# Kernel optimization log

Measured on AMD Instinct MI355X. Metric: run time of the kernel, lower is better.

Reference implementation:

```python
import jax, jax.numpy as jnp
import numpy as np

B = 8192
N_COLS = 64
D = 1024
EPS = 1e-5


def _layernorm(x, g, b):
    m = jnp.mean(x, axis=-1, keepdims=True)
    v = jnp.mean(jnp.square(x - m), axis=-1, keepdims=True)
    return (x - m) * jax.lax.rsqrt(v + EPS) * g + b


def setup_inputs() -> dict:
    key = jax.random.key(0)
    ks = jax.random.split(key, 8)
    s = 0.02
    return {
        "x1_enc": jax.random.normal(ks[0], (1, N_COLS, D), jnp.float32),
        "x2_enc": jax.random.normal(ks[1], (B, D), jnp.float32),
        "We": jax.random.normal(ks[2], (4, 2 * D, D), jnp.float32) * s,
        "be": jnp.zeros((4, D), jnp.float32),
        "W1": jax.random.normal(ks[3], (2 * D, 4 * D), jnp.float32) * s,
        "b1": jnp.zeros((4 * D,), jnp.float32),
        "g1": jnp.ones((4 * D,), jnp.float32),
        "bt1": jnp.zeros((4 * D,), jnp.float32),
        "W2": jax.random.normal(ks[4], (4 * D, 2 * D), jnp.float32) * s,
        "b2": jnp.zeros((2 * D,), jnp.float32),
        "g2": jnp.ones((2 * D,), jnp.float32),
        "bt2": jnp.zeros((2 * D,), jnp.float32),
        "W3": jax.random.normal(ks[5], (2 * D, 1), jnp.float32) * s,
        "b3": jnp.zeros((1,), jnp.float32),
        "col_pairs": jax.random.randint(ks[6], (B, 2), 0, N_COLS, jnp.int64),
        "vis_type": jax.random.randint(ks[7], (B,), 0, 4, jnp.int64),
    }


def reference(x1_enc, x2_enc, We, be, W1, b1, g1, bt1, W2, b2, g2, bt2, W3, b3,
              col_pairs, vis_type):
    # x1 repeated B times is identical per row -> gather directly from x1_enc[0]
    x11 = x1_enc[0, col_pairs[:, 0]]          # [B, D]
    x12 = x1_enc[0, col_pairs[:, 1]]          # [B, D]
    x1c = jnp.concatenate([x11, x12], axis=1)  # [B, 2D]

    # 1-of-4 expert routing: compute all experts, select by vis_type
    all_y = jax.nn.relu(jnp.einsum('bd,edk->bek', x1c, We) + be)  # [B, 4, D]
    y1 = jnp.take_along_axis(all_y, vis_type[:, None, None], axis=1)[:, 0]  # [B, D]

    y = jnp.concatenate([y1, x2_enc], axis=1)  # [B, 2D]
    h = _layernorm(jax.nn.relu(y @ W1 + b1), g1, bt1)
    h = _layernorm(jax.nn.relu(h @ W2 + b2), g2, bt2)
    return jax.nn.sigmoid(h @ W3 + b3)  # [B, 1]
```

## Files before the change

kernel.cpp:

```cpp
#include <hip/hip_runtime.h>

typedef unsigned short u16;
typedef __bf16 bf16x8 __attribute__((ext_vector_type(8)));
typedef float f32x4v __attribute__((ext_vector_type(4)));
typedef u16 u16x8 __attribute__((ext_vector_type(8)));

__device__ __forceinline__ u16 f2bf(float f) {
  union { float f; unsigned u; } v; v.f = f;
  unsigned r = v.u + 0x7fffu + ((v.u >> 16) & 1u);
  return (u16)(r >> 16);
}
__device__ __forceinline__ float bf2f(u16 h) {
  union { unsigned u; float f; } v; v.u = ((unsigned)h) << 16;
  return v.f;
}

#define G2L16(g, l)                                                            \
  __builtin_amdgcn_global_load_lds((__attribute__((address_space(1))) void*)(g), \
                                   (__attribute__((address_space(3))) void*)(l), 16, 0, 0)

__global__ __launch_bounds__(256) void k_transpose2(const float* __restrict__ W1,
                                                    u16* __restrict__ W1T,
                                                    const float* __restrict__ W2,
                                                    u16* __restrict__ W2gT,
                                                    const float* __restrict__ g1) {
  __shared__ float tile[64][65];
  int bid = blockIdx.x;
  const float* in;
  u16* out;
  int R, C, bx, by, fold;
  if (bid < 2048) {
    in = W1; out = W1T; R = 2048; C = 4096; fold = 0;
    bx = bid & 63; by = bid >> 6;
  } else {
    bid -= 2048;
    in = W2; out = W2gT; R = 4096; C = 2048; fold = 1;
    bx = bid & 31; by = bid >> 5;
  }
  const int c0 = bx * 64, r0 = by * 64;
  const int tc = (threadIdx.x & 15) * 4, tr = threadIdx.x >> 4;
#pragma unroll
  for (int i = 0; i < 4; ++i) {
    int r = tr + i * 16;
    f32x4v v = *(const f32x4v*)(in + (size_t)(r0 + r) * C + c0 + tc);
    tile[r][tc] = v[0]; tile[r][tc + 1] = v[1];
    tile[r][tc + 2] = v[2]; tile[r][tc + 3] = v[3];
  }
  __syncthreads();
  const int oc = threadIdx.x >> 2;
  const int rb = (threadIdx.x & 3) * 16;
  float gv[16];
#pragma unroll
  for (int i = 0; i < 16; ++i) gv[i] = fold ? g1[r0 + rb + i] : 1.f;
  u16x8 o0, o1;
#pragma unroll
  for (int i = 0; i < 8; ++i) o0[i] = f2bf(tile[rb + i][oc] * gv[i]);
#pragma unroll
  for (int i = 0; i < 8; ++i) o1[i] = f2bf(tile[rb + 8 + i][oc] * gv[8 + i]);
  *(u16x8*)(out + (size_t)(c0 + oc) * R + r0 + rb) = o0;
  *(u16x8*)(out + (size_t)(c0 + oc) * R + r0 + rb + 8) = o1;
}

__global__ __launch_bounds__(256) void k_pq(const float* __restrict__ x1,
                                            const float* __restrict__ We,
                                            float* __restrict__ pq0,
                                            float* __restrict__ pq1) {
  const int n0 = blockIdx.x * 64;
  const int ep = blockIdx.y;
  const int e = ep >> 1, p = ep & 1;
  const int ks = blockIdx.z * 512;
  float* pq = blockIdx.z ? pq1 : pq0;
  __shared__ float As[64][33];
  __shared__ float Bs[32][68];
  const int t = threadIdx.x;
  const int tx = t & 15, ty = t >> 4;
  float acc[4][4] = {};
  const float* wbase = We + (size_t)e * 2048 * 1024 + (size_t)p * 1024 * 1024;
  for (int k0 = ks; k0 < ks + 512; k0 += 32) {
#pragma unroll
    for (int i = 0; i < 8; ++i) {
      int idx = t + i * 256;
      As[idx >> 5][idx & 31] = x1[(size_t)(idx >> 5) * 1024 + k0 + (idx & 31)];
    }
#pragma unroll
    for (int i = 0; i < 8; ++i) {
      int idx = t + i * 256;
      Bs[idx >> 6][idx & 63] = wbase[(size_t)(k0 + (idx >> 6)) * 1024 + n0 + (idx & 63)];
    }
    __syncthreads();
#pragma unroll
    for (int kk = 0; kk < 32; ++kk) {
      float av[4];
#pragma unroll
      for (int i = 0; i < 4; ++i) av[i] = As[ty * 4 + i][kk];
      f32x4v bv = *(const f32x4v*)&Bs[kk][tx * 4];
#pragma unroll
      for (int i = 0; i < 4; ++i)
#pragma unroll
        for (int j = 0; j < 4; ++j) acc[i][j] += av[i] * bv[j];
    }
    __syncthreads();
  }
#pragma unroll
  for (int i = 0; i < 4; ++i) {
    float* dst = pq + ((size_t)ep * 64 + ty * 4 + i) * 1024 + n0 + tx * 4;
#pragma unroll
    for (int j = 0; j < 4; ++j) dst[j] = acc[i][j];
  }
}

__global__ __launch_bounds__(256) void k_w2vec(const float* __restrict__ W2,
                                               const float* __restrict__ g1,
                                               const float* __restrict__ bt1,
                                               const float* __restrict__ b2,
                                               float* __restrict__ s1,
                                               float* __restrict__ c1b) {
  const int n = blockIdx.x * 256 + threadIdx.x;
  const int ks = blockIdx.y * 256;
  float s = 0.f, c = 0.f;
  for (int k = ks; k < ks + 256; ++k) {
    float w = W2[(size_t)k * 2048 + n];
    s += g1[k] * w;
    c += bt1[k] * w;
  }
  if (blockIdx.y == 0) c += b2[n];
  atomicAdd(&s1[n], s);
  atomicAdd(&c1b[n], c);
}

__global__ __launch_bounds__(256) void k_build_y(const float* __restrict__ pq0,
                                                 const float* __restrict__ pq1,
                                                 const float* __restrict__ x2,
                                                 const float* __restrict__ be,
                                                 const int* __restrict__ cp,
                                                 const int* __restrict__ vis,
                                                 u16* __restrict__ Y) {
  const int b = blockIdx.x;
  const int t = threadIdx.x;
  const int e = vis[b];
  u16x8 o;
  if (t < 128) {
    const int c0 = cp[2 * b], c1 = cp[2 * b + 1];
    const size_t po = ((size_t)(e * 2) * 64 + c0) * 1024 + t * 8;
    const size_t qo = ((size_t)(e * 2 + 1) * 64 + c1) * 1024 + t * 8;
    const float* B = be + e * 1024 + t * 8;
#pragma unroll
    for (int i = 0; i < 8; ++i) {
      float v = pq0[po + i] + pq1[po + i] + pq0[qo + i] + pq1[qo + i] + B[i];
      o[i] = f2bf(v > 0.f ? v : 0.f);
    }
    *(u16x8*)(Y + (size_t)b * 2048 + t * 8) = o;
  } else {
    const float* X = x2 + (size_t)b * 1024 + (size_t)(t - 128) * 8;
#pragma unroll
    for (int i = 0; i < 8; ++i) o[i] = f2bf(X[i]);
    *(u16x8*)(Y + (size_t)b * 2048 + 1024 + (size_t)(t - 128) * 8) = o;
  }
}

template <int MODE>
__global__ __launch_bounds__(256, 4) void k_gemm(const u16* __restrict__ A,
                                                 const u16* __restrict__ BT,
                                                 const float* __restrict__ bias,
                                                 const float2* __restrict__ stats,
                                                 const float* __restrict__ s1,
                                                 const float* __restrict__ c1b,
                                                 u16* __restrict__ C, int M, int N, int K) {
  __shared__ u16 As[128 * 64];
  __shared__ u16 Bs[128 * 64];
  const int tid = threadIdx.x;
  const int lane = tid & 63;
  const int wave = tid >> 6;

  const int nx = gridDim.x, ny = gridDim.y;
  const int bid = blockIdx.y * nx + blockIdx.x;
  const int stripe = ny >> 3;
  const int xcd = bid & 7;
  const int loc = bid >> 3;
  const int panel = loc / (stripe * 4);
  const int rem = loc - panel * (stripe * 4);
  const int by = xcd * stripe + (rem >> 2);
  const int bx = panel * 4 + (rem & 3);
  const int tileN = bx * 128;
  const int tileM = by * 128;
  const int wm = wave & 1;
  const int wn = wave >> 1;

  f32x4v acc[4][4];
#pragma unroll
  for (int i = 0; i < 4; ++i)
#pragma unroll
    for (int j = 0; j < 4; ++j) acc[i][j] = (f32x4v){0.f, 0.f, 0.f, 0.f};

  const int srow = tid >> 3;
  const int lchunk = (tid & 7) ^ (srow & 7);
  const u16* aptr = A + (size_t)(tileM + srow) * K + lchunk * 8;
  const u16* bptr = BT + (size_t)(tileN + srow) * K + lchunk * 8;
  u16* asp = As + tid * 8;
  u16* bsp = Bs + tid * 8;

  const int s = lane & 7;
  const int kp0 = ((lane >> 4) ^ s) * 8;
  const int kp1 = kp0 ^ 32;
  const int am = wm * 64 + (lane & 15);
  const int bn = wn * 64 + (lane & 15);

  for (int k0 = 0; k0 < K; k0 += 64) {
    G2L16(aptr, asp);
    G2L16(aptr + (size_t)32 * K, asp + 2048);
    G2L16(aptr + (size_t)64 * K, asp + 4096);
    G2L16(aptr + (size_t)96 * K, asp + 6144);
    G2L16(bptr, bsp);
    G2L16(bptr + (size_t)32 * K, bsp + 2048);
    G2L16(bptr + (size_t)64 * K, bsp + 4096);
    G2L16(bptr + (size_t)96 * K, bsp + 6144);
    aptr += 64;
    bptr += 64;
    __syncthreads();

    bf16x8 af[4], bfr[4];
#pragma unroll
    for (int mi = 0; mi < 4; ++mi)
      af[mi] = *(const bf16x8*)(As + (am + mi * 16) * 64 + kp0);
#pragma unroll
    for (int ni = 0; ni < 4; ++ni)
      bfr[ni] = *(const bf16x8*)(Bs + (bn + ni * 16) * 64 + kp0);
#pragma unroll
    for (int mi = 0; mi < 4; ++mi)
#pragma unroll
      for (int ni = 0; ni < 4; ++ni)
        acc[mi][ni] = __builtin_amdgcn_mfma_f32_16x16x32_bf16(af[mi], bfr[ni], acc[mi][ni], 0, 0, 0);
#pragma unroll
    for (int mi = 0; mi < 4; ++mi)
      af[mi] = *(const bf16x8*)(As + (am + mi * 16) * 64 + kp1);
#pragma unroll
    for (int ni = 0; ni < 4; ++ni)
      bfr[ni] = *(const bf16x8*)(Bs + (bn + ni * 16) * 64 + kp1);
#pragma unroll
    for (int mi = 0; mi < 4; ++mi)
#pragma unroll
      for (int ni = 0; ni < 4; ++ni)
        acc[mi][ni] = __builtin_amdgcn_mfma_f32_16x16x32_bf16(af[mi], bfr[ni], acc[mi][ni], 0, 0, 0);
    __syncthreads();
  }

  const int crow = tileM + wm * 64 + (lane >> 4) * 4;
  const int ccol = tileN + wn * 64 + (lane & 15);
  float cv0[4], cv1[4];
#pragma unroll
  for (int ni = 0; ni < 4; ++ni) {
    const int c = ccol + ni * 16;
    if (MODE == 0) {
      cv0[ni] = bias[c];
    } else {
      cv0[ni] = s1[c];
      cv1[ni] = c1b[c];
    }
  }
#pragma unroll
  for (int mi = 0; mi < 4; ++mi) {
#pragma unroll
    for (int r = 0; r < 4; ++r) {
      const int row = crow + mi * 16 + r;
      float m = 0.f, rs = 0.f;
      if (MODE == 1) {
        float2 st = stats[row];
        m = st.x; rs = st.y;
      }
#pragma unroll
      for (int ni = 0; ni < 4; ++ni) {
        float v;
        if (MODE == 0)
          v = acc[mi][ni][r] + cv0[ni];
        else
          v = rs * acc[mi][ni][r] - rs * m * cv0[ni] + cv1[ni];
        v = v > 0.f ? v : 0.f;
        C[(size_t)row * N + ccol + ni * 16] = f2bf(v);
      }
    }
  }
}

__global__ __launch_bounds__(256) void k_stats(const u16* __restrict__ H1,
                                               float2* __restrict__ stats) {
  const u16* row = H1 + (size_t)blockIdx.x * 4096;
  const int t = threadIdx.x;
  float s = 0.f, ss = 0.f;
#pragma unroll
  for (int j = 0; j < 2; ++j) {
    u16x8 v = *(const u16x8*)(row + j * 2048 + t * 8);
#pragma unroll
    for (int i = 0; i < 8; ++i) {
      float f = bf2f(v[i]);
      s += f;
      ss += f * f;
    }
  }
#pragma unroll
  for (int off = 32; off > 0; off >>= 1) {
    s += __shfl_down(s, off, 64);
    ss += __shfl_down(ss, off, 64);
  }
  __shared__ float red[8];
  const int lane = t & 63, wv = t >> 6;
  if (lane == 0) { red[wv] = s; red[4 + wv] = ss; }
  __syncthreads();
  if (t == 0) {
    float S = red[0] + red[1] + red[2] + red[3];
    float SS = red[4] + red[5] + red[6] + red[7];
    float m = S * (1.f / 4096.f);
    float var = SS * (1.f / 4096.f) - m * m;
    stats[blockIdx.x] = make_float2(m, rsqrtf(var + 1e-5f));
  }
}

__global__ __launch_bounds__(256) void k_ln_final(const u16* __restrict__ H2,
                                                  const float* __restrict__ g,
                                                  const float* __restrict__ bt,
                                                  const float* __restrict__ W3,
                                                  const float* __restrict__ b3,
                                                  float* __restrict__ out) {
  const int b = blockIdx.x, t = threadIdx.x;
  const u16* row = H2 + (size_t)b * 2048;
  float vals[8];
  float s = 0.f, ss = 0.f;
  {
    u16x8 v = *(const u16x8*)(row + t * 8);
#pragma unroll
    for (int i = 0; i < 8; ++i) {
      float f = bf2f(v[i]);
      vals[i] = f;
      s += f;
      ss += f * f;
    }
  }
#pragma unroll
  for (int off = 32; off > 0; off >>= 1) {
    s += __shfl_down(s, off, 64);
    ss += __shfl_down(ss, off, 64);
  }
  __shared__ float red[8];
  const int lane = t & 63, wv = t >> 6;
  if (lane == 0) { red[wv] = s; red[4 + wv] = ss; }
  __syncthreads();
  if (t == 0) {
    float S = red[0] + red[1] + red[2] + red[3];
    float SS = red[4] + red[5] + red[6] + red[7];
    float m = S * (1.f / 2048.f);
    float var = SS * (1.f / 2048.f) - m * m;
    red[0] = m;
    red[1] = rsqrtf(var + 1e-5f);
  }
  __syncthreads();
  const float m = red[0], rs = red[1];
  float dot = 0.f;
#pragma unroll
  for (int i = 0; i < 8; ++i) {
    int col = t * 8 + i;
    float h = (vals[i] - m) * rs * g[col] + bt[col];
    dot += h * W3[col];
  }
#pragma unroll
  for (int off = 32; off > 0; off >>= 1) dot += __shfl_down(dot, off, 64);
  __syncthreads();
  if (lane == 0) red[wv] = dot;
  __syncthreads();
  if (t == 0) {
    float S = red[0] + red[1] + red[2] + red[3] + b3[0];
    out[b] = 1.f / (1.f + expf(-S));
  }
}

extern "C" void kernel_launch(void* const* d_in, const int* in_sizes, int n_in,
                              void* d_out, int out_size, void* d_ws, size_t ws_size,
                              hipStream_t stream) {
  const float* x1 = (const float*)d_in[0];
  const float* x2 = (const float*)d_in[1];
  const float* We = (const float*)d_in[2];
  const float* be = (const float*)d_in[3];
  const float* W1 = (const float*)d_in[4];
  const float* b1 = (const float*)d_in[5];
  const float* g1 = (const float*)d_in[6];
  const float* bt1 = (const float*)d_in[7];
  const float* W2 = (const float*)d_in[8];
  const float* b2 = (const float*)d_in[9];
  const float* g2 = (const float*)d_in[10];
  const float* bt2 = (const float*)d_in[11];
  const float* W3 = (const float*)d_in[12];
  const float* b3 = (const float*)d_in[13];
  const int* cp = (const int*)d_in[14];
  const int* vis = (const int*)d_in[15];
  float* out = (float*)d_out;

  char* ws = (char*)d_ws;
  u16* W1T  = (u16*)(ws);
  u16* W2gT = (u16*)(ws + 16777216);
  u16* Y    = (u16*)(ws + 33554432);
  u16* H1   = (u16*)(ws + 67108864);
  float* PQ0 = (float*)(ws + 134217728);
  float* PQ1 = (float*)(ws + 136314880);
  float2* stats = (float2*)(ws + 138412032);
  float* s1  = (float*)(ws + 138477568);
  float* c1b = (float*)(ws + 138485760);
  u16* H2 = Y;

  hipMemsetAsync(s1, 0, 2 * 2048 * sizeof(float), stream);
  k_transpose2<<<4096, 256, 0, stream>>>(W1, W1T, W2, W2gT, g1);
  k_pq<<<dim3(16, 8, 2), 256, 0, stream>>>(x1, We, PQ0, PQ1);
  k_w2vec<<<dim3(8, 16), 256, 0, stream>>>(W2, g1, bt1, b2, s1, c1b);
  k_build_y<<<8192, 256, 0, stream>>>(PQ0, PQ1, x2, be, cp, vis, Y);
  k_gemm<0><<<dim3(4096 / 128, 8192 / 128), 256, 0, stream>>>(
      Y, W1T, b1, nullptr, nullptr, nullptr, H1, 8192, 4096, 2048);
  k_stats<<<8192, 256, 0, stream>>>(H1, stats);
  k_gemm<1><<<dim3(2048 / 128, 8192 / 128), 256, 0, stream>>>(
      H1, W2gT, nullptr, stats, s1, c1b, H2, 8192, 2048, 4096);
  k_ln_final<<<8192, 256, 0, stream>>>(H2, g2, bt2, W3, b3, out);
}
```

Before: 491.7 us.

## Double-buffer GEMM LDS, fuse LN1 stats and W2 vector sums into producers

The GEMM main loop now uses two LDS buffers, so the next K-tile's global-to-LDS loads are in flight while the current tile is computed. This halves the barriers per tile but doubles shared memory, and the occupancy hint is dropped. Row sum and sum-of-squares for the first layernorm are computed in the GEMM0 epilogue and reduced by a small kernel, replacing the separate pass over H1. The W2·g1 and W2·bt1 vector products are folded into the transpose kernel, and build_y and ln_final process several rows per block with wave-level reductions.

```diff
diff --git a/kernel.cpp b/kernel.cpp
--- a/kernel.cpp
+++ b/kernel.cpp
@@ -23,7 +23,10 @@
                                                     u16* __restrict__ W1T,
                                                     const float* __restrict__ W2,
                                                     u16* __restrict__ W2gT,
-                                                    const float* __restrict__ g1) {
+                                                    const float* __restrict__ g1,
+                                                    const float* __restrict__ bt1,
+                                                    float* __restrict__ w2ps,
+                                                    float* __restrict__ w2pc) {
   __shared__ float tile[64][65];
   int bid = blockIdx.x;
   const float* in;
@@ -38,7 +41,8 @@
     bx = bid & 31; by = bid >> 5;
   }
   const int c0 = bx * 64, r0 = by * 64;
-  const int tc = (threadIdx.x & 15) * 4, tr = threadIdx.x >> 4;
+  const int t = threadIdx.x;
+  const int tc = (t & 15) * 4, tr = t >> 4;
 #pragma unroll
   for (int i = 0; i < 4; ++i) {
     int r = tr + i * 16;
@@ -47,8 +51,8 @@
     tile[r][tc + 2] = v[2]; tile[r][tc + 3] = v[3];
   }
   __syncthreads();
-  const int oc = threadIdx.x >> 2;
-  const int rb = (threadIdx.x & 3) * 16;
+  const int oc = t >> 2;
+  const int rb = (t & 3) * 16;
   float gv[16];
 #pragma unroll
   for (int i = 0; i < 16; ++i) gv[i] = fold ? g1[r0 + rb + i] : 1.f;
@@ -59,6 +63,21 @@
   for (int i = 0; i < 8; ++i) o1[i] = f2bf(tile[rb + 8 + i][oc] * gv[8 + i]);
   *(u16x8*)(out + (size_t)(c0 + oc) * R + r0 + rb) = o0;
   *(u16x8*)(out + (size_t)(c0 + oc) * R + r0 + rb + 8) = o1;
+  if (fold) {
+    float ps = 0.f, pc = 0.f;
+#pragma unroll
+    for (int i = 0; i < 16; ++i) {
+      float w = tile[rb + i][oc];
+      ps += gv[i] * w;
+      pc += bt1[r0 + rb + i] * w;
+    }
+    ps += __shfl_down(ps, 2, 4); ps += __shfl_down(ps, 1, 4);
+    pc += __shfl_down(pc, 2, 4); pc += __shfl_down(pc, 1, 4);
+    if ((t & 3) == 0) {
+      w2ps[(size_t)by * 2048 + c0 + oc] = ps;
+      w2pc[(size_t)by * 2048 + c0 + oc] = pc;
+    }
+  }
 }
 
 __global__ __launch_bounds__(256) void k_pq(const float* __restrict__ x1,
@@ -109,25 +128,6 @@
   }
 }
 
-__global__ __launch_bounds__(256) void k_w2vec(const float* __restrict__ W2,
-                                               const float* __restrict__ g1,
-                                               const float* __restrict__ bt1,
-                                               const float* __restrict__ b2,
-                                               float* __restrict__ s1,
-                                               float* __restrict__ c1b) {
-  const int n = blockIdx.x * 256 + threadIdx.x;
-  const int ks = blockIdx.y * 256;
-  float s = 0.f, c = 0.f;
-  for (int k = ks; k < ks + 256; ++k) {
-    float w = W2[(size_t)k * 2048 + n];
-    s += g1[k] * w;
-    c += bt1[k] * w;
-  }
-  if (blockIdx.y == 0) c += b2[n];
-  atomicAdd(&s1[n], s);
-  atomicAdd(&c1b[n], c);
-}
-
 __global__ __launch_bounds__(256) void k_build_y(const float* __restrict__ pq0,
                                                  const float* __restrict__ pq1,
                                                  const float* __restrict__ x2,
@@ -135,39 +135,78 @@
                                                  const int* __restrict__ cp,
                                                  const int* __restrict__ vis,
                                                  u16* __restrict__ Y) {
-  const int b = blockIdx.x;
   const int t = threadIdx.x;
-  const int e = vis[b];
-  u16x8 o;
-  if (t < 128) {
-    const int c0 = cp[2 * b], c1 = cp[2 * b + 1];
-    const size_t po = ((size_t)(e * 2) * 64 + c0) * 1024 + t * 8;
-    const size_t qo = ((size_t)(e * 2 + 1) * 64 + c1) * 1024 + t * 8;
-    const float* B = be + e * 1024 + t * 8;
-#pragma unroll
-    for (int i = 0; i < 8; ++i) {
-      float v = pq0[po + i] + pq1[po + i] + pq0[qo + i] + pq1[qo + i] + B[i];
-      o[i] = f2bf(v > 0.f ? v : 0.f);
-    }
-    *(u16x8*)(Y + (size_t)b * 2048 + t * 8) = o;
-  } else {
-    const float* X = x2 + (size_t)b * 1024 + (size_t)(t - 128) * 8;
-#pragma unroll
-    for (int i = 0; i < 8; ++i) o[i] = f2bf(X[i]);
-    *(u16x8*)(Y + (size_t)b * 2048 + 1024 + (size_t)(t - 128) * 8) = o;
-  }
-}
+  for (int rr = 0; rr < 8; ++rr) {
+    const int b = blockIdx.x * 8 + rr;
+    const int e = vis[b];
+    u16x8 o;
+    if (t < 128) {
+      const int c0 = cp[2 * b], c1 = cp[2 * b + 1];
+      const size_t po = ((size_t)(e * 2) * 64 + c0) * 1024 + t * 8;
+      const size_t qo = ((size_t)(e * 2 + 1) * 64 + c1) * 1024 + t * 8;
+      const float* B = be + e * 1024 + t * 8;
+#pragma unroll
+      for (int i = 0; i < 8; ++i) {
+        float v = pq0[po + i] + pq1[po + i] + pq0[qo + i] + pq1[qo + i] + B[i];
+        o[i] = f2bf(v > 0.f ? v : 0.f);
+      }
+      *(u16x8*)(Y + (size_t)b * 2048 + t * 8) = o;
+    } else {
+      const float* X = x2 + (size_t)b * 1024 + (size_t)(t - 128) * 8;
+#pragma unroll
+      for (int i = 0; i < 8; ++i) o[i] = f2bf(X[i]);
+      *(u16x8*)(Y + (size_t)b * 2048 + 1024 + (size_t)(t - 128) * 8) = o;
+    }
+  }
+}
+
+#define LOADAB(ASP, BSP)                                                       \
+  {                                                                            \
+    G2L16(aA, (ASP));                                                          \
+    G2L16(aA + (size_t)32 * K, (ASP) + 2048);                                  \
+    G2L16(aA + (size_t)64 * K, (ASP) + 4096);                                  \
+    G2L16(aA + (size_t)96 * K, (ASP) + 6144);                                  \
+    G2L16(bB, (BSP));                                                          \
+    G2L16(bB + (size_t)32 * K, (BSP) + 2048);                                  \
+    G2L16(bB + (size_t)64 * K, (BSP) + 4096);                                  \
+    G2L16(bB + (size_t)96 * K, (BSP) + 6144);                                  \
+    aA += 64; bB += 64;                                                        \
+  }
+
+#define COMPUTE(ASB, BSB)                                                      \
+  {                                                                            \
+    bf16x8 af[4], bfr[4];                                                      \
+    _Pragma("unroll") for (int mi = 0; mi < 4; ++mi)                           \
+        af[mi] = *(const bf16x8*)((ASB) + (am + mi * 16) * 64 + kp0);          \
+    _Pragma("unroll") for (int ni = 0; ni < 4; ++ni)                           \
+        bfr[ni] = *(const bf16x8*)((BSB) + (bn + ni * 16) * 64 + kp0);         \
+    _Pragma("unroll") for (int mi = 0; mi < 4; ++mi)                           \
+        _Pragma("unroll") for (int ni = 0; ni < 4; ++ni)                       \
+            acc[mi][ni] = __builtin_amdgcn_mfma_f32_16x16x32_bf16(             \
+                af[mi], bfr[ni], acc[mi][ni], 0, 0, 0);                        \
+    _Pragma("unroll") for (int mi = 0; mi < 4; ++mi)                           \
+        af[mi] = *(const bf16x8*)((ASB) + (am + mi * 16) * 64 + kp1);          \
+    _Pragma("unroll") for (int ni = 0; ni < 4; ++ni)                           \
+        bfr[ni] = *(const bf16x8*)((BSB) + (bn + ni * 16) * 64 + kp1);         \
+    _Pragma("unroll") for (int mi = 0; mi < 4; ++mi)                           \
+        _Pragma("unroll") for (int ni = 0; ni < 4; ++ni)                       \
+            acc[mi][ni] = __builtin_amdgcn_mfma_f32_16x16x32_bf16(             \
+                af[mi], bfr[ni], acc[mi][ni], 0, 0, 0);                        \
+  }
 
 template <int MODE>
-__global__ __launch_bounds__(256, 4) void k_gemm(const u16* __restrict__ A,
-                                                 const u16* __restrict__ BT,
-                                                 const float* __restrict__ bias,
-                                                 const float2* __restrict__ stats,
-                                                 const float* __restrict__ s1,
-                                                 const float* __restrict__ c1b,
-                                                 u16* __restrict__ C, int M, int N, int K) {
-  __shared__ u16 As[128 * 64];
-  __shared__ u16 Bs[128 * 64];
+__global__ __launch_bounds__(256) void k_gemm(const u16* __restrict__ A,
+                                              const u16* __restrict__ BT,
+                                              const float* __restrict__ bias,
+                                              const float2* __restrict__ stats,
+                                              const float* __restrict__ s1,
+                                              const float* __restrict__ c1b,
+                                              float2* __restrict__ sp_out,
+                                              u16* __restrict__ C, int M, int N, int K) {
+  __shared__ u16 As0[128 * 64];
+  __shared__ u16 As1[128 * 64];
+  __shared__ u16 Bs0[128 * 64];
+  __shared__ u16 Bs1[128 * 64];
   const int tid = threadIdx.x;
   const int lane = tid & 63;
   const int wave = tid >> 6;
@@ -194,10 +233,12 @@
 
   const int srow = tid >> 3;
   const int lchunk = (tid & 7) ^ (srow & 7);
-  const u16* aptr = A + (size_t)(tileM + srow) * K + lchunk * 8;
-  const u16* bptr = BT + (size_t)(tileN + srow) * K + lchunk * 8;
-  u16* asp = As + tid * 8;
-  u16* bsp = Bs + tid * 8;
+  const u16* aA = A + (size_t)(tileM + srow) * K + lchunk * 8;
+  const u16* bB = BT + (size_t)(tileN + srow) * K + lchunk * 8;
+  u16* asp0 = As0 + tid * 8;
+  u16* asp1 = As1 + tid * 8;
+  u16* bsp0 = Bs0 + tid * 8;
+  u16* bsp1 = Bs1 + tid * 8;
 
   const int s = lane & 7;
   const int kp0 = ((lane >> 4) ^ s) * 8;
@@ -205,42 +246,15 @@
   const int am = wm * 64 + (lane & 15);
   const int bn = wn * 64 + (lane & 15);
 
-  for (int k0 = 0; k0 < K; k0 += 64) {
-    G2L16(aptr, asp);
-    G2L16(aptr + (size_t)32 * K, asp + 2048);
-    G2L16(aptr + (size_t)64 * K, asp + 4096);
-    G2L16(aptr + (size_t)96 * K, asp + 6144);
-    G2L16(bptr, bsp);
-    G2L16(bptr + (size_t)32 * K, bsp + 2048);
-    G2L16(bptr + (size_t)64 * K, bsp + 4096);
-    G2L16(bptr + (size_t)96 * K, bsp + 6144);
-    aptr += 64;
-    bptr += 64;
+  const int n = K >> 6;
+  LOADAB(asp0, bsp0);
+  __syncthreads();
+  for (int it = 0; it < n; it += 2) {
+    LOADAB(asp1, bsp1);
+    COMPUTE(As0, Bs0);
     __syncthreads();
-
-    bf16x8 af[4], bfr[4];
-#pragma unroll
-    for (int mi = 0; mi < 4; ++mi)
-      af[mi] = *(const bf16x8*)(As + (am + mi * 16) * 64 + kp0);
-#pragma unroll
-    for (int ni = 0; ni < 4; ++ni)
-      bfr[ni] = *(const bf16x8*)(Bs + (bn + ni * 16) * 64 + kp0);
-#pragma unroll
-    for (int mi = 0; mi < 4; ++mi)
-#pragma unroll
-      for (int ni = 0; ni < 4; ++ni)
-        acc[mi][ni] = __builtin_amdgcn_mfma_f32_16x16x32_bf16(af[mi], bfr[ni], acc[mi][ni], 0, 0, 0);
-#pragma unroll
-    for (int mi = 0; mi < 4; ++mi)
-      af[mi] = *(const bf16x8*)(As + (am + mi * 16) * 64 + kp1);
-#pragma unroll
-    for (int ni = 0; ni < 4; ++ni)
-      bfr[ni] = *(const bf16x8*)(Bs + (bn + ni * 16) * 64 + kp1);
-#pragma unroll
-    for (int mi = 0; mi < 4; ++mi)
-#pragma unroll
-      for (int ni = 0; ni < 4; ++ni)
-        acc[mi][ni] = __builtin_amdgcn_mfma_f32_16x16x32_bf16(af[mi], bfr[ni], acc[mi][ni], 0, 0, 0);
+    if (it + 2 < n) LOADAB(asp0, bsp0);
+    COMPUTE(As1, Bs1);
     __syncthreads();
   }
 
@@ -257,6 +271,7 @@
       cv1[ni] = c1b[c];
     }
   }
+  const int cb = bx * 2 + wn;
 #pragma unroll
   for (int mi = 0; mi < 4; ++mi) {
 #pragma unroll
@@ -267,6 +282,7 @@
         float2 st = stats[row];
         m = st.x; rs = st.y;
       }
+      float s_ = 0.f, ss_ = 0.f;
 #pragma unroll
       for (int ni = 0; ni < 4; ++ni) {
         float v;
@@ -275,42 +291,49 @@
         else
           v = rs * acc[mi][ni][r] - rs * m * cv0[ni] + cv1[ni];
         v = v > 0.f ? v : 0.f;
+        if (MODE == 0) { s_ += v; ss_ += v * v; }
         C[(size_t)row * N + ccol + ni * 16] = f2bf(v);
       }
-    }
-  }
-}
-
-__global__ __launch_bounds__(256) void k_stats(const u16* __restrict__ H1,
-                                               float2* __restrict__ stats) {
-  const u16* row = H1 + (size_t)blockIdx.x * 4096;
-  const int t = threadIdx.x;
-  float s = 0.f, ss = 0.f;
-#pragma unroll
-  for (int j = 0; j < 2; ++j) {
-    u16x8 v = *(const u16x8*)(row + j * 2048 + t * 8);
-#pragma unroll
-    for (int i = 0; i < 8; ++i) {
-      float f = bf2f(v[i]);
-      s += f;
-      ss += f * f;
-    }
-  }
-#pragma unroll
-  for (int off = 32; off > 0; off >>= 1) {
-    s += __shfl_down(s, off, 64);
-    ss += __shfl_down(ss, off, 64);
-  }
-  __shared__ float red[8];
-  const int lane = t & 63, wv = t >> 6;
-  if (lane == 0) { red[wv] = s; red[4 + wv] = ss; }
-  __syncthreads();
-  if (t == 0) {
-    float S = red[0] + red[1] + red[2] + red[3];
-    float SS = red[4] + red[5] + red[6] + red[7];
-    float m = S * (1.f / 4096.f);
-    float var = SS * (1.f / 4096.f) - m * m;
-    stats[blockIdx.x] = make_float2(m, rsqrtf(var + 1e-5f));
+      if (MODE == 0) {
+#pragma unroll
+        for (int off = 8; off >= 1; off >>= 1) {
+          s_ += __shfl_xor(s_, off, 16);
+          ss_ += __shfl_xor(ss_, off, 16);
+        }
+        if ((lane & 15) == 0)
+          sp_out[(size_t)cb * 8192 + row] = make_float2(s_, ss_);
+      }
+    }
+  }
+}
+
+__global__ __launch_bounds__(256) void k_reduce(const float2* __restrict__ sp,
+                                                float2* __restrict__ stats,
+                                                const float* __restrict__ w2ps,
+                                                const float* __restrict__ w2pc,
+                                                const float* __restrict__ b2,
+                                                float* __restrict__ s1,
+                                                float* __restrict__ c1b) {
+  const int bid = blockIdx.x;
+  if (bid < 32) {
+    const int row = bid * 256 + threadIdx.x;
+    float s = 0.f, ss = 0.f;
+    for (int cbk = 0; cbk < 64; ++cbk) {
+      float2 p = sp[(size_t)cbk * 8192 + row];
+      s += p.x; ss += p.y;
+    }
+    float m = s * (1.f / 4096.f);
+    float var = ss * (1.f / 4096.f) - m * m;
+    stats[row] = make_float2(m, rsqrtf(var + 1e-5f));
+  } else {
+    const int nn = (bid - 32) * 256 + threadIdx.x;
+    float s = 0.f, c = 0.f;
+    for (int kb = 0; kb < 64; ++kb) {
+      s += w2ps[(size_t)kb * 2048 + nn];
+      c += w2pc[(size_t)kb * 2048 + nn];
+    }
+    s1[nn] = s;
+    c1b[nn] = c + b2[nn];
   }
 }
 
@@ -320,16 +343,18 @@
                                                   const float* __restrict__ W3,
                                                   const float* __restrict__ b3,
                                                   float* __restrict__ out) {
-  const int b = blockIdx.x, t = threadIdx.x;
+  const int lane = threadIdx.x & 63;
+  const int b = blockIdx.x * 4 + (threadIdx.x >> 6);
   const u16* row = H2 + (size_t)b * 2048;
-  float vals[8];
+  float vals[4][8];
   float s = 0.f, ss = 0.f;
-  {
-    u16x8 v = *(const u16x8*)(row + t * 8);
+#pragma unroll
+  for (int c = 0; c < 4; ++c) {
+    u16x8 v = *(const u16x8*)(row + c * 512 + lane * 8);
 #pragma unroll
     for (int i = 0; i < 8; ++i) {
       float f = bf2f(v[i]);
-      vals[i] = f;
+      vals[c][i] = f;
       s += f;
       ss += f * f;
     }
@@ -339,36 +364,22 @@
     s += __shfl_down(s, off, 64);
     ss += __shfl_down(ss, off, 64);
   }
-  __shared__ float red[8];
-  const int lane = t & 63, wv = t >> 6;
-  if (lane == 0) { red[wv] = s; red[4 + wv] = ss; }
-  __syncthreads();
-  if (t == 0) {
-    float S = red[0] + red[1] + red[2] + red[3];
-    float SS = red[4] + red[5] + red[6] + red[7];
-    float m = S * (1.f / 2048.f);
-    float var = SS * (1.f / 2048.f) - m * m;
-    red[0] = m;
-    red[1] = rsqrtf(var + 1e-5f);
-  }
-  __syncthreads();
-  const float m = red[0], rs = red[1];
+  s = __shfl(s, 0);
+  ss = __shfl(ss, 0);
+  const float m = s * (1.f / 2048.f);
+  const float rs = rsqrtf(ss * (1.f / 2048.f) - m * m + 1e-5f);
   float dot = 0.f;
 #pragma unroll
-  for (int i = 0; i < 8; ++i) {
-    int col = t * 8 + i;
-    float h = (vals[i] - m) * rs * g[col] + bt[col];
-    dot += h * W3[col];
-  }
+  for (int c = 0; c < 4; ++c)
+#pragma unroll
+    for (int i = 0; i < 8; ++i) {
+      int col = c * 512 + lane * 8 + i;
+      float h = (vals[c][i] - m) * rs * g[col] + bt[col];
+      dot += h * W3[col];
+    }
 #pragma unroll
   for (int off = 32; off > 0; off >>= 1) dot += __shfl_down(dot, off, 64);
-  __syncthreads();
-  if (lane == 0) red[wv] = dot;
-  __syncthreads();
-  if (t == 0) {
-    float S = red[0] + red[1] + red[2] + red[3] + b3[0];
-    out[b] = 1.f / (1.f + expf(-S));
-  }
+  if (lane == 0) out[b] = 1.f / (1.f + expf(-(dot + b3[0])));
 }
 
 extern "C" void kernel_launch(void* const* d_in, const int* in_sizes, int n_in,
@@ -399,20 +410,21 @@
   u16* H1   = (u16*)(ws + 67108864);
   float* PQ0 = (float*)(ws + 134217728);
   float* PQ1 = (float*)(ws + 136314880);
+  float2* sp = (float2*)(ws + 134217728);
   float2* stats = (float2*)(ws + 138412032);
-  float* s1  = (float*)(ws + 138477568);
-  float* c1b = (float*)(ws + 138485760);
+  float* s1   = (float*)(ws + 138477568);
+  float* c1b  = (float*)(ws + 138485760);
+  float* w2ps = (float*)(ws + 138493952);
+  float* w2pc = (float*)(ws + 139018240);
   u16* H2 = Y;
 
-  hipMemsetAsync(s1, 0, 2 * 2048 * sizeof(float), stream);
-  k_transpose2<<<4096, 256, 0, stream>>>(W1, W1T, W2, W2gT, g1);
+  k_transpose2<<<4096, 256, 0, stream>>>(W1, W1T, W2, W2gT, g1, bt1, w2ps, w2pc);
   k_pq<<<dim3(16, 8, 2), 256, 0, stream>>>(x1, We, PQ0, PQ1);
-  k_w2vec<<<dim3(8, 16), 256, 0, stream>>>(W2, g1, bt1, b2, s1, c1b);
-  k_build_y<<<8192, 256, 0, stream>>>(PQ0, PQ1, x2, be, cp, vis, Y);
-  k_gemm<0><<<dim3(4096 / 128, 8192 / 128), 256, 0, stream>>>(
-      Y, W1T, b1, nullptr, nullptr, nullptr, H1, 8192, 4096, 2048);
-  k_stats<<<8192, 256, 0, stream>>>(H1, stats);
-  k_gemm<1><<<dim3(2048 / 128, 8192 / 128), 256, 0, stream>>>(
-      H1, W2gT, nullptr, stats, s1, c1b, H2, 8192, 2048, 4096);
-  k_ln_final<<<8192, 256, 0, stream>>>(H2, g2, bt2, W3, b3, out);
-}
+  k_build_y<<<1024, 256, 0, stream>>>(PQ0, PQ1, x2, be, cp, vis, Y);
+  k_gemm<0><<<dim3(32, 64), 256, 0, stream>>>(
+      Y, W1T, b1, nullptr, nullptr, nullptr, sp, H1, 8192, 4096, 2048);
+  k_reduce<<<40, 256, 0, stream>>>(sp, stats, w2ps, w2pc, b2, s1, c1b);
+  k_gemm<1><<<dim3(16, 64), 256, 0, stream>>>(
+      H1, W2gT, nullptr, stats, s1, c1b, nullptr, H2, 8192, 2048, 4096);
+  k_ln_final<<<2048, 256, 0, stream>>>(H2, g2, bt2, W3, b3, out);
+}
```

Measured after the change: 508.3 us. 3.4% more time.
